# Kernel tuning notes

Hardware: AMD Instinct MI355X
Metric: run time of the kernel (lower is better)

## Reference

```python
import jax, jax.numpy as jnp
import numpy as np


def setup_inputs() -> dict:
    key = jax.random.key(0)
    kx, kw = jax.random.split(key)
    B, IN, OUT = 8192, 1024, 4096
    x = jax.random.normal(kx, (B, IN), dtype=jnp.float32)
    # torch.rand -> uniform [0,1)
    weight = jax.random.uniform(kw, (IN, OUT), dtype=jnp.float32)
    return {"x": x, "weight": weight}


def reference(x, weight):
    # Faithful to: (x.unsqueeze(-1) - weight).pow(2).sum(-2)
    # i.e. out[b, o] = sum_i (x[b, i] - weight[i, o])**2
    # Computed via the squared-distance expansion to avoid the
    # (B, in, out) broadcast intermediate:
    x_sq = jnp.sum(x * x, axis=-1, keepdims=True)          # (B, 1)
    w_sq = jnp.sum(weight * weight, axis=0)                # (OUT,)
    cross = jnp.matmul(x, weight)                          # (B, OUT)
    return x_sq - 2.0 * cross + w_sq
```

## Files before the change

### kernel.cpp

```cpp
#include <hip/hip_runtime.h>
#include <cstdint>
#include <cstddef>

#define B_DIM   8192
#define IN_DIM  1024
#define OUT_DIM 4096
#define KT2     (IN_DIM / 64)

typedef __attribute__((ext_vector_type(8)))  int   i32x8;
typedef __attribute__((ext_vector_type(4)))  int   i32x4;
typedef __attribute__((ext_vector_type(16))) float f32x16;

__device__ __forceinline__ void async_copy16(const void* gptr, void* ldsptr) {
    __builtin_amdgcn_global_load_lds(
        (__attribute__((address_space(1))) void*)gptr,
        (__attribute__((address_space(3))) void*)ldsptr,
        16, 0, 0);
}

__device__ __forceinline__ int pack4_fp8(float a, float b, float c, float d) {
    int pk = __builtin_amdgcn_cvt_pk_fp8_f32(a, b, 0, false);
    pk = __builtin_amdgcn_cvt_pk_fp8_f32(c, d, pk, true);
    return pk;
}


__global__ __launch_bounds__(256) void tile_x_kernel(
    const float* __restrict__ x, unsigned char* __restrict__ At,
    float* __restrict__ xsq, float* __restrict__ wsq)
{
    const int t = threadIdx.x;
    const int w = t >> 6;
    const int l = t & 63;
    const int mt = blockIdx.x;
    const int m  = mt * 32 + (l & 31);

    float s = 0.0f;
    #pragma unroll
    for (int c = 0; c < 4; ++c) {
        const int kt2 = c * 4 + w;
        const float* src = x + (size_t)m * IN_DIM + kt2 * 64 + (l >> 5) * 32;
        i32x4 lo, hi;
        #pragma unroll
        for (int j = 0; j < 4; ++j) {
            float4 v = ((const float4*)src)[j];
            s += v.x*v.x + v.y*v.y + v.z*v.z + v.w*v.w;
            lo[j] = pack4_fp8(v.x, v.y, v.z, v.w);
        }
        #pragma unroll
        for (int j = 0; j < 4; ++j) {
            float4 v = ((const float4*)src)[4 + j];
            s += v.x*v.x + v.y*v.y + v.z*v.z + v.w*v.w;
            hi[j] = pack4_fp8(v.x, v.y, v.z, v.w);
        }
        unsigned char* pan = At + ((size_t)mt * KT2 + kt2) * 2048;
        *(i32x4*)(pan + l * 16)        = lo;
        *(i32x4*)(pan + 1024 + l * 16) = hi;
    }
    s += __shfl_down(s, 32, 64);
    __shared__ float red[4][32];
    if (l < 32) red[w][l] = s;
    __syncthreads();
    if (t < 32) xsq[mt * 32 + t] = red[0][t] + red[1][t] + red[2][t] + red[3][t];

    if (blockIdx.x < OUT_DIM / 256) wsq[blockIdx.x * 256 + t] = 0.0f;
}

__global__ __launch_bounds__(256) void tile_w_kernel(
    const float* __restrict__ wgt, unsigned char* __restrict__ Bt,
    float* __restrict__ wsq)
{
    __shared__ float tile[256 * 33];
    const int t  = threadIdx.x;
    const int w  = t >> 6;
    const int l  = t & 63;
    const int nt = blockIdx.x;
    const int q  = blockIdx.y;
    const int n0 = nt * 32;

    {
        const int rbase = t >> 2, cg = (t & 3) * 8;
        #pragma unroll
        for (int rep = 0; rep < 4; ++rep) {
            const int r = rbase + rep * 64;
            const float* src = wgt + (size_t)(q * 256 + r) * OUT_DIM + n0 + cg;
            float4 v0 = ((const float4*)src)[0];
            float4 v1 = ((const float4*)src)[1];
            float* d = &tile[r * 33 + cg];
            d[0] = v0.x; d[1] = v0.y; d[2] = v0.z; d[3] = v0.w;
            d[4] = v1.x; d[5] = v1.y; d[6] = v1.z; d[7] = v1.w;
        }
    }
    __syncthreads();

    const int kt2 = q * 4 + w;
    const int n   = l & 31;
    const int kb  = w * 64 + (l >> 5) * 32;
    float s = 0.0f;
    i32x4 lo, hi;
    #pragma unroll
    for (int j4 = 0; j4 < 4; ++j4) {
        float f0 = tile[(kb + j4 * 4 + 0) * 33 + n];
        float f1 = tile[(kb + j4 * 4 + 1) * 33 + n];
        float f2 = tile[(kb + j4 * 4 + 2) * 33 + n];
        float f3 = tile[(kb + j4 * 4 + 3) * 33 + n];
        s += f0*f0 + f1*f1 + f2*f2 + f3*f3;
        lo[j4] = pack4_fp8(f0, f1, f2, f3);
    }
    #pragma unroll
    for (int j4 = 0; j4 < 4; ++j4) {
        float f0 = tile[(kb + 16 + j4 * 4 + 0) * 33 + n];
        float f1 = tile[(kb + 16 + j4 * 4 + 1) * 33 + n];
        float f2 = tile[(kb + 16 + j4 * 4 + 2) * 33 + n];
        float f3 = tile[(kb + 16 + j4 * 4 + 3) * 33 + n];
        s += f0*f0 + f1*f1 + f2*f2 + f3*f3;
        hi[j4] = pack4_fp8(f0, f1, f2, f3);
    }
    unsigned char* pan = Bt + ((size_t)nt * KT2 + kt2) * 2048;
    *(i32x4*)(pan + l * 16)        = lo;
    *(i32x4*)(pan + 1024 + l * 16) = hi;

    s += __shfl_down(s, 32, 64);
    __shared__ float red[4][32];
    if (l < 32) red[w][l] = s;
    __syncthreads();
    if (t < 32) atomicAdd(&wsq[n0 + t], red[0][t] + red[1][t] + red[2][t] + red[3][t]);
}

__global__ __launch_bounds__(256) void rbf_gemm_kernel(
    const unsigned char* __restrict__ At,
    const unsigned char* __restrict__ Bt,
    const float* __restrict__ xsq,
    const float* __restrict__ wsq,
    float* __restrict__ out)
{
    __shared__ __align__(16) unsigned char sm[2][32768];

    const int t    = threadIdx.x;
    const int w    = t >> 6;
    const int l    = t & 63;
    const int l32  = l & 31;
    const int half = l >> 5;
    const int bm = blockIdx.x;
    const int bn = blockIdx.y;
    const int waveRow = w >> 1;
    const int waveCol = w & 1;

    f32x16 acc[2][2];
    #pragma unroll
    for (int mi = 0; mi < 2; ++mi)
        #pragma unroll
        for (int ni = 0; ni < 2; ++ni)
            #pragma unroll
            for (int r = 0; r < 16; ++r)
                acc[mi][ni][r] = 0.0f;

    auto stage = [&](int buf, int kti) {
        unsigned char* As = sm[buf];
        unsigned char* Bs = sm[buf] + 16384;
        #pragma unroll
        for (int pp = 0; pp < 2; ++pp) {
            const int p = w * 2 + pp;
            const unsigned char* ga = At + ((size_t)(bm * 4 + w) * KT2 + kti * 2 + pp) * 2048;
            const unsigned char* gb = Bt + ((size_t)(bn * 4 + w) * KT2 + kti * 2 + pp) * 2048;
            #pragma unroll
            for (int h = 0; h < 2; ++h) {
                async_copy16(ga + h * 1024 + l * 16, As + p * 2048 + h * 1024);
                async_copy16(gb + h * 1024 + l * 16, Bs + p * 2048 + h * 1024);
            }
        }
    };

    auto ldfrag = [&](const unsigned char* base, int p) -> i32x8 {
        i32x4 lo = *(const i32x4*)(base + p * 2048 + l * 16);
        i32x4 hi = *(const i32x4*)(base + p * 2048 + 1024 + l * 16);
        i32x8 r;
        r[0] = lo[0]; r[1] = lo[1]; r[2] = lo[2]; r[3] = lo[3];
        r[4] = hi[0]; r[5] = hi[1]; r[6] = hi[2]; r[7] = hi[3];
        return r;
    };

    stage(0, 0);
    __syncthreads();

    for (int kti = 0; kti < 8; ++kti) {
        if (kti < 7) stage((kti + 1) & 1, kti + 1);

        const unsigned char* As = sm[kti & 1];
        const unsigned char* Bs = sm[kti & 1] + 16384;
        #pragma unroll
        for (int ks = 0; ks < 2; ++ks) {
            i32x8 af[2], bf[2];
            #pragma unroll
            for (int mi = 0; mi < 2; ++mi)
                af[mi] = ldfrag(As, (waveRow * 2 + mi) * 2 + ks);
            #pragma unroll
            for (int ni = 0; ni < 2; ++ni)
                bf[ni] = ldfrag(Bs, (waveCol * 2 + ni) * 2 + ks);
            #pragma unroll
            for (int mi = 0; mi < 2; ++mi)
                #pragma unroll
                for (int ni = 0; ni < 2; ++ni)
                    acc[mi][ni] = __builtin_amdgcn_mfma_scale_f32_32x32x64_f8f6f4(
                        af[mi], bf[ni], acc[mi][ni],
                        0, 0,
                        0, 0x7F7F7F7F,
                        0, 0x7F7F7F7F);
        }
        __syncthreads();
    }

    #pragma unroll
    for (int mi = 0; mi < 2; ++mi) {
        const int mbase = bm * 128 + waveRow * 64 + mi * 32 + 4 * half;
        #pragma unroll
        for (int r2 = 0; r2 < 4; ++r2) {
            #pragma unroll
            for (int r1 = 0; r1 < 4; ++r1) {
                const int m  = mbase + r1 + 8 * r2;
                const float xs = xsq[m];
                #pragma unroll
                for (int ni = 0; ni < 2; ++ni) {
                    const int n = bn * 128 + waveCol * 64 + ni * 32 + l32;
                    out[(size_t)m * OUT_DIM + n] =
                        xs + wsq[n] - 2.0f * acc[mi][ni][r2 * 4 + r1];
                }
            }
        }
    }
}

extern "C" void kernel_launch(void* const* d_in, const int* in_sizes, int n_in,
                              void* d_out, int out_size, void* d_ws, size_t ws_size,
                              hipStream_t stream)
{
    const float* x   = (const float*)d_in[0];
    const float* wgt = (const float*)d_in[1];
    float* out = (float*)d_out;
    char*  ws  = (char*)d_ws;

    unsigned char* At = (unsigned char*)ws;
    unsigned char* Bt = (unsigned char*)(ws + (size_t)B_DIM * IN_DIM);
    float* xsq = (float*)(ws + (size_t)B_DIM * IN_DIM + (size_t)OUT_DIM * IN_DIM);
    float* wsq = xsq + B_DIM;

    tile_x_kernel<<<B_DIM / 32, 256, 0, stream>>>(x, At, xsq, wsq);
    tile_w_kernel<<<dim3(OUT_DIM / 32, 4), 256, 0, stream>>>(wgt, Bt, wsq);
    rbf_gemm_kernel<<<dim3(B_DIM / 128, OUT_DIM / 128), 256, 0, stream>>>(At, Bt, xsq, wsq, out);
}
```

Baseline: 201.1 us.

## Enlarge FP8 GEMM tile to 256x256 with triple-buffered LDS and grid swizzle

The GEMM moves from 128x128 tiles with 4 waves to 256x256 tiles with 8 waves, each wave computing a 128x64 subtile. The K loop now uses a three-deep LDS ring with explicit vmcnt waits and raw barriers, raises wave priority around the MFMA block, and remaps workgroups so neighbouring groups share tiles in cache. The x-tiling kernel is changed to 512 threads. The goal is more operand reuse per byte loaded, better latency hiding and better L2 locality, at the cost of fewer workgroups (512), higher register use and 96KB of LDS per block.

```diff
diff --git a/kernel.cpp b/kernel.cpp
--- a/kernel.cpp
+++ b/kernel.cpp
@@ -25,7 +25,7 @@
 }
 
 
-__global__ __launch_bounds__(256) void tile_x_kernel(
+__global__ __launch_bounds__(512) void tile_x_kernel(
     const float* __restrict__ x, unsigned char* __restrict__ At,
     float* __restrict__ xsq, float* __restrict__ wsq)
 {
@@ -37,8 +37,8 @@
 
     float s = 0.0f;
     #pragma unroll
-    for (int c = 0; c < 4; ++c) {
-        const int kt2 = c * 4 + w;
+    for (int c = 0; c < 2; ++c) {
+        const int kt2 = c * 8 + w;
         const float* src = x + (size_t)m * IN_DIM + kt2 * 64 + (l >> 5) * 32;
         i32x4 lo, hi;
         #pragma unroll
@@ -58,12 +58,17 @@
         *(i32x4*)(pan + 1024 + l * 16) = hi;
     }
     s += __shfl_down(s, 32, 64);
-    __shared__ float red[4][32];
+    __shared__ float red[8][32];
     if (l < 32) red[w][l] = s;
     __syncthreads();
-    if (t < 32) xsq[mt * 32 + t] = red[0][t] + red[1][t] + red[2][t] + red[3][t];
-
-    if (blockIdx.x < OUT_DIM / 256) wsq[blockIdx.x * 256 + t] = 0.0f;
+    if (t < 32) {
+        float r = 0.0f;
+        #pragma unroll
+        for (int j = 0; j < 8; ++j) r += red[j][t];
+        xsq[mt * 32 + t] = r;
+    }
+
+    if (blockIdx.x < 8) wsq[blockIdx.x * 512 + t] = 0.0f;
 }
 
 __global__ __launch_bounds__(256) void tile_w_kernel(
@@ -127,47 +132,49 @@
     if (t < 32) atomicAdd(&wsq[n0 + t], red[0][t] + red[1][t] + red[2][t] + red[3][t]);
 }
 
-__global__ __launch_bounds__(256) void rbf_gemm_kernel(
+__global__ __launch_bounds__(512, 2) void rbf_gemm_kernel(
     const unsigned char* __restrict__ At,
     const unsigned char* __restrict__ Bt,
     const float* __restrict__ xsq,
     const float* __restrict__ wsq,
     float* __restrict__ out)
 {
-    __shared__ __align__(16) unsigned char sm[2][32768];
+    __shared__ __align__(16) unsigned char sm[3][32768];
 
     const int t    = threadIdx.x;
     const int w    = t >> 6;
     const int l    = t & 63;
     const int l32  = l & 31;
     const int half = l >> 5;
-    const int bm = blockIdx.x;
-    const int bn = blockIdx.y;
-    const int waveRow = w >> 1;
-    const int waveCol = w & 1;
-
-    f32x16 acc[2][2];
-    #pragma unroll
-    for (int mi = 0; mi < 2; ++mi)
+    const int waveRow = w >> 2;
+    const int waveCol = w & 3;
+
+    const int wg  = blockIdx.y * 32 + blockIdx.x;
+    const int swz = (wg & 7) * 64 + (wg >> 3);
+    const int bm  = swz >> 4;
+    const int bn  = swz & 15;
+
+    f32x16 acc[4][2];
+    #pragma unroll
+    for (int mi = 0; mi < 4; ++mi)
         #pragma unroll
         for (int ni = 0; ni < 2; ++ni)
             #pragma unroll
             for (int r = 0; r < 16; ++r)
                 acc[mi][ni][r] = 0.0f;
 
-    auto stage = [&](int buf, int kti) {
-        unsigned char* As = sm[buf];
-        unsigned char* Bs = sm[buf] + 16384;
-        #pragma unroll
-        for (int pp = 0; pp < 2; ++pp) {
-            const int p = w * 2 + pp;
-            const unsigned char* ga = At + ((size_t)(bm * 4 + w) * KT2 + kti * 2 + pp) * 2048;
-            const unsigned char* gb = Bt + ((size_t)(bn * 4 + w) * KT2 + kti * 2 + pp) * 2048;
-            #pragma unroll
-            for (int h = 0; h < 2; ++h) {
-                async_copy16(ga + h * 1024 + l * 16, As + p * 2048 + h * 1024);
-                async_copy16(gb + h * 1024 + l * 16, Bs + p * 2048 + h * 1024);
-            }
+    const unsigned char* gaBase = At + (size_t)(bm * 8 + w) * (KT2 * 2048);
+    const unsigned char* gbBase = Bt + (size_t)(bn * 8 + w) * (KT2 * 2048);
+
+    auto stage = [&](unsigned char* base, int k) {
+        const unsigned char* ga = gaBase + k * 2048;
+        const unsigned char* gb = gbBase + k * 2048;
+        unsigned char* As = base + w * 2048;
+        unsigned char* Bs = base + 16384 + w * 2048;
+        #pragma unroll
+        for (int h = 0; h < 2; ++h) {
+            async_copy16(ga + h * 1024 + l * 16, As + h * 1024);
+            async_copy16(gb + h * 1024 + l * 16, Bs + h * 1024);
         }
     };
 
@@ -180,51 +187,60 @@
         return r;
     };
 
-    stage(0, 0);
-    __syncthreads();
-
-    for (int kti = 0; kti < 8; ++kti) {
-        if (kti < 7) stage((kti + 1) & 1, kti + 1);
-
-        const unsigned char* As = sm[kti & 1];
-        const unsigned char* Bs = sm[kti & 1] + 16384;
-        #pragma unroll
-        for (int ks = 0; ks < 2; ++ks) {
-            i32x8 af[2], bf[2];
-            #pragma unroll
-            for (int mi = 0; mi < 2; ++mi)
-                af[mi] = ldfrag(As, (waveRow * 2 + mi) * 2 + ks);
-            #pragma unroll
-            for (int ni = 0; ni < 2; ++ni)
-                bf[ni] = ldfrag(Bs, (waveCol * 2 + ni) * 2 + ks);
-            #pragma unroll
-            for (int mi = 0; mi < 2; ++mi)
-                #pragma unroll
-                for (int ni = 0; ni < 2; ++ni)
-                    acc[mi][ni] = __builtin_amdgcn_mfma_scale_f32_32x32x64_f8f6f4(
-                        af[mi], bf[ni], acc[mi][ni],
-                        0, 0,
-                        0, 0x7F7F7F7F,
-                        0, 0x7F7F7F7F);
-        }
-        __syncthreads();
-    }
-
-    #pragma unroll
-    for (int mi = 0; mi < 2; ++mi) {
-        const int mbase = bm * 128 + waveRow * 64 + mi * 32 + 4 * half;
+    stage(sm[0], 0);
+    stage(sm[1], 1);
+
+    int cb = 0, sb = 2;
+    for (int k = 0; k < 16; ++k) {
+        if (k < 15) asm volatile("s_waitcnt vmcnt(4)" ::: "memory");
+        else        asm volatile("s_waitcnt vmcnt(0)" ::: "memory");
+        __builtin_amdgcn_s_barrier();
+        __builtin_amdgcn_sched_barrier(0);
+
+        if (k <= 13) stage(sm[sb], k + 2);
+
+        const unsigned char* As = sm[cb];
+        const unsigned char* Bs = sm[cb] + 16384;
+        i32x8 bf0 = ldfrag(Bs, waveCol * 2 + 0);
+        i32x8 bf1 = ldfrag(Bs, waveCol * 2 + 1);
+        i32x8 af[4];
+        #pragma unroll
+        for (int mi = 0; mi < 4; ++mi)
+            af[mi] = ldfrag(As, waveRow * 4 + mi);
+
+        __builtin_amdgcn_s_setprio(1);
+        #pragma unroll
+        for (int mi = 0; mi < 4; ++mi) {
+            acc[mi][0] = __builtin_amdgcn_mfma_scale_f32_32x32x64_f8f6f4(
+                af[mi], bf0, acc[mi][0],
+                0, 0,
+                0, 0x7F7F7F7F,
+                0, 0x7F7F7F7F);
+            acc[mi][1] = __builtin_amdgcn_mfma_scale_f32_32x32x64_f8f6f4(
+                af[mi], bf1, acc[mi][1],
+                0, 0, 0, 0x7F7F7F7F, 0, 0x7F7F7F7F);
+        }
+        __builtin_amdgcn_s_setprio(0);
+
+        cb = (cb == 2) ? 0 : cb + 1;
+        sb = (sb == 2) ? 0 : sb + 1;
+    }
+
+    const int ncol = bn * 256 + waveCol * 64 + l32;
+    const float wsn0 = wsq[ncol];
+    const float wsn1 = wsq[ncol + 32];
+    #pragma unroll
+    for (int mi = 0; mi < 4; ++mi) {
+        const int mbase = bm * 256 + waveRow * 128 + mi * 32 + 4 * half;
         #pragma unroll
         for (int r2 = 0; r2 < 4; ++r2) {
             #pragma unroll
             for (int r1 = 0; r1 < 4; ++r1) {
                 const int m  = mbase + r1 + 8 * r2;
                 const float xs = xsq[m];
-                #pragma unroll
-                for (int ni = 0; ni < 2; ++ni) {
-                    const int n = bn * 128 + waveCol * 64 + ni * 32 + l32;
-                    out[(size_t)m * OUT_DIM + n] =
-                        xs + wsq[n] - 2.0f * acc[mi][ni][r2 * 4 + r1];
-                }
+                float* orow = out + (size_t)m * OUT_DIM + ncol;
+                orow[0]  = xs + wsn0 - 2.0f * acc[mi][0][r2 * 4 + r1];
+                orow[32] = xs + wsn1 - 2.0f * acc[mi][1][r2 * 4 + r1];
             }
         }
     }
@@ -244,7 +260,7 @@
     float* xsq = (float*)(ws + (size_t)B_DIM * IN_DIM + (size_t)OUT_DIM * IN_DIM);
     float* wsq = xsq + B_DIM;
 
-    tile_x_kernel<<<B_DIM / 32, 256, 0, stream>>>(x, At, xsq, wsq);
+    tile_x_kernel<<<B_DIM / 32, 512, 0, stream>>>(x, At, xsq, wsq);
     tile_w_kernel<<<dim3(OUT_DIM / 32, 4), 256, 0, stream>>>(wgt, Bt, wsq);
-    rbf_gemm_kernel<<<dim3(B_DIM / 128, OUT_DIM / 128), 256, 0, stream>>>(At, Bt, xsq, wsq, out);
-}
+    rbf_gemm_kernel<<<dim3(32, 16), 512, 0, stream>>>(At, Bt, xsq, wsq, out);
+}
```

Result: no change. 197.6 us (-1.7%).
